# Optimization experiments

Measured on AMD Instinct MI355X. Metric: run time of the kernel, lower is better.

Reference implementation:

```python
import jax, jax.numpy as jnp
import numpy as np

N_NODES = 100000
N_EDGES = 600000
HID = 128
CH_OUT = 3


def setup_inputs() -> dict:
    key = jax.random.key(0)
    ks = jax.random.split(key, 16)
    s = 0.05  # small init to keep tanh in its linear-ish range
    inp = {
        "x": jax.random.normal(ks[0], (N_NODES, HID), dtype=jnp.float32),
        "pos": jax.random.normal(ks[1], (N_NODES, 3), dtype=jnp.float32),
        "edge_index": jax.random.randint(ks[2], (2, N_EDGES), 0, N_NODES, dtype=jnp.int32),
        "fe_w1": jax.random.normal(ks[3], (2 * HID + 1, HID), dtype=jnp.float32) * s,
        "fe_b1": jnp.zeros((HID,), jnp.float32),
        "fe_w2": jax.random.normal(ks[4], (HID, HID), dtype=jnp.float32) * s,
        "fe_b2": jnp.zeros((HID,), jnp.float32),
        "finf_w": jax.random.normal(ks[5], (HID, 1), dtype=jnp.float32) * s,
        "finf_b": jnp.zeros((1,), jnp.float32),
        "fh_w1": jax.random.normal(ks[6], (2 * HID, HID), dtype=jnp.float32) * s,
        "fh_b1": jnp.zeros((HID,), jnp.float32),
        "fh_w2": jax.random.normal(ks[7], (HID, HID), dtype=jnp.float32) * s,
        "fh_b2": jnp.zeros((HID,), jnp.float32),
        "l1_w": jax.random.normal(ks[8], (HID, HID), dtype=jnp.float32) * s,
        "l1_b": jnp.zeros((HID,), jnp.float32),
        "l2_w": jax.random.normal(ks[9], (HID, HID), dtype=jnp.float32) * s,
        "l2_b": jnp.zeros((HID,), jnp.float32),
        "l3_w": jax.random.normal(ks[10], (HID, HID), dtype=jnp.float32) * s,
        "l3_b": jnp.zeros((HID,), jnp.float32),
        "l4_w": jax.random.normal(ks[11], (HID, HID), dtype=jnp.float32) * s,
        "l4_b": jnp.zeros((HID,), jnp.float32),
        "l5_w": jax.random.normal(ks[12], (HID, CH_OUT), dtype=jnp.float32) * s,
        "l5_b": jnp.zeros((CH_OUT,), jnp.float32),
    }
    return inp


def reference(x, pos, edge_index, fe_w1, fe_b1, fe_w2, fe_b2, finf_w, finf_b,
              fh_w1, fh_b1, fh_w2, fh_b2, l1_w, l1_b, l2_w, l2_b, l3_w, l3_b,
              l4_w, l4_b, l5_w, l5_b):
    e_st, e_end = edge_index[0], edge_index[1]
    # dists = ||(pos_i - pos_j)^2||_2  (norm of the squared difference, as in source)
    d = pos[e_st] - pos[e_end]                                  # [E, 3]
    dists = jnp.linalg.norm(jnp.square(d), axis=1, keepdims=True)  # [E, 1]
    # edge MLP f_e
    tmp = jnp.concatenate([x[e_st], x[e_end], dists], axis=1)   # [E, 2H+1]
    m_ij = jnp.tanh(tmp @ fe_w1 + fe_b1)
    m_ij = jnp.tanh(m_ij @ fe_w2 + fe_b2)                        # [E, H]
    # gating f_inf
    e_ij = jnp.tanh(m_ij @ finf_w + finf_b)                      # [E, 1]
    # scatter-sum to source nodes (index_add on edge_index[0])
    m_i = jax.ops.segment_sum(e_ij * m_ij, e_st, num_segments=x.shape[0])  # [N, H]
    # node update f_h with residual
    h = jnp.concatenate([x, m_i], axis=1)                        # [N, 2H]
    x = x + (jnp.tanh(h @ fh_w1 + fh_b1) @ fh_w2 + fh_b2)
    # dense head (dropout p=0.0 is identity)
    lrelu = lambda v: jax.nn.leaky_relu(v, negative_slope=0.01)
    x = lrelu(x @ l1_w + l1_b)
    x = lrelu(x @ l2_w + l2_b)
    x = lrelu(x @ l3_w + l3_b)
    x = lrelu(x @ l4_w + l4_b)
    return x @ l5_w + l5_b
```

## Files before the change

kernel.cpp:

```cpp
#include <hip/hip_runtime.h>
#include <math.h>

#define HID 128

typedef unsigned short u16;
typedef __attribute__((ext_vector_type(8))) short bfrag;
typedef __attribute__((ext_vector_type(4))) float f32x4;
typedef __attribute__((ext_vector_type(8))) unsigned short u16x8;
typedef __attribute__((ext_vector_type(4))) unsigned short u16x4;

__device__ __forceinline__ float fast_tanh(float v) {
    v = fminf(15.0f, fmaxf(-15.0f, v));
    float e = __expf(2.0f * v);
    float r = __builtin_amdgcn_rcpf(e + 1.0f);
    return 1.0f - 2.0f * r;
}

__device__ __forceinline__ u16 f2b(float f) {
    union { float f; unsigned int u; } v;
    v.f = f;
    unsigned int u = v.u;
    return (u16)((u + 0x7FFFu + ((u >> 16) & 1u)) >> 16);
}
__device__ __forceinline__ float b2f(u16 b) {
    union { unsigned int u; float f; } v;
    v.u = ((unsigned int)b) << 16;
    return v.f;
}
__device__ __forceinline__ float bits2f(unsigned u) {
    union { unsigned u; float f; } v; v.u = u; return v.f;
}

__global__ void __launch_bounds__(256) prep_x(const float* __restrict__ x,
                                              u16* __restrict__ xb) {
    int i = blockIdx.x * 256 + threadIdx.x;
    const float4 v0 = *(const float4*)(x + (size_t)i * 8);
    const float4 v1 = *(const float4*)(x + (size_t)i * 8 + 4);
    u16x8 o = { f2b(v0.x), f2b(v0.y), f2b(v0.z), f2b(v0.w),
                f2b(v1.x), f2b(v1.y), f2b(v1.z), f2b(v1.w) };
    *(u16x8*)(xb + (size_t)i * 8) = o;
}

__global__ void __launch_bounds__(256) prep_weights(
    const float* __restrict__ w1, const float* __restrict__ fh1,
    const float* __restrict__ w2, const float* __restrict__ fh2,
    const float* __restrict__ l1, const float* __restrict__ l2,
    const float* __restrict__ l3, const float* __restrict__ l4,
    u16* __restrict__ w1t, u16* __restrict__ fh1t,
    u16* __restrict__ w2t, u16* __restrict__ fh2t,
    u16* __restrict__ l1t, u16* __restrict__ l2t,
    u16* __restrict__ l3t, u16* __restrict__ l4t)
{
    int b = blockIdx.x, t = threadIdx.x;
    const float* src; u16* dst; int K;
    if (b < 256) {
        K = 256;
        if (b < 128) { src = w1;  dst = w1t; }
        else         { src = fh1; dst = fh1t; b -= 128; }
    } else {
        K = 128;
        int s = (b - 256) >> 6; b = (b - 256) & 63;
        switch (s) {
            case 0:  src = w2;  dst = w2t;  break;
            case 1:  src = fh2; dst = fh2t; break;
            case 2:  src = l1;  dst = l1t;  break;
            case 3:  src = l2;  dst = l2t;  break;
            case 4:  src = l3;  dst = l3t;  break;
            default: src = l4;  dst = l4t;  break;
        }
    }
    int idx = b * 256 + t;
    int k = idx >> 7, n = idx & 127;
    dst[(size_t)n * K + k] = f2b(src[(size_t)k * 128 + n]);
}

__global__ void __launch_bounds__(256) hist_kernel(const int* __restrict__ est,
                                                   int* __restrict__ cnt, int E) {
    int e = blockIdx.x * 256 + threadIdx.x;
    if (e < E) atomicAdd(&cnt[est[e]], 1);
}

__global__ void __launch_bounds__(256) scan1(const int* __restrict__ cnt,
                                             int* __restrict__ scanout,
                                             int* __restrict__ partial, int N) {
    __shared__ int s[256];
    int t = threadIdx.x, b = blockIdx.x, i = b * 256 + t;
    int v = (i < N) ? cnt[i] : 0;
    s[t] = v; __syncthreads();
#pragma unroll
    for (int d = 1; d < 256; d <<= 1) {
        int add = (t >= d) ? s[t - d] : 0;
        __syncthreads();
        s[t] += add;
        __syncthreads();
    }
    if (i < N) scanout[i] = s[t] - v;
    if (t == 255) partial[b] = s[255];
}

__global__ void __launch_bounds__(512) scan2(int* __restrict__ partial, int NB) {
    __shared__ int s[512];
    int t = threadIdx.x;
    int v = (t < NB) ? partial[t] : 0;
    s[t] = v; __syncthreads();
#pragma unroll
    for (int d = 1; d < 512; d <<= 1) {
        int add = (t >= d) ? s[t - d] : 0;
        __syncthreads();
        s[t] += add;
        __syncthreads();
    }
    if (t < NB) partial[t] = s[t] - v;
}

__global__ void __launch_bounds__(256) scan3(const int* __restrict__ scanout,
                                             const int* __restrict__ partial,
                                             int* __restrict__ offs,
                                             int* __restrict__ cur, int N, int E) {
    int t = threadIdx.x, b = blockIdx.x, i = b * 256 + t;
    if (i < N) { int o = scanout[i] + partial[b]; offs[i] = o; cur[i] = o; }
    if (i == 0) offs[N] = E;
}

__global__ void __launch_bounds__(256) reorder_kernel(const int* __restrict__ est,
                                                      const int* __restrict__ eend,
                                                      int* __restrict__ cur,
                                                      int* __restrict__ est_s,
                                                      int* __restrict__ eend_s, int E) {
    int e = blockIdx.x * 256 + threadIdx.x;
    if (e < E) {
        int s = est[e];
        int p = atomicAdd(&cur[s], 1);
        est_s[p]  = s;
        eend_s[p] = eend[e];
    }
}

template<int KD>
__device__ __forceinline__ void gemm_k(const u16* sbuf, const u16* __restrict__ wt,
                                       int w, int l16, int l4g, f32x4 (&acc)[2][2]) {
    const int RS = KD * 2;
#pragma unroll
    for (int k0 = 0; k0 < KD; k0 += 32) {
        const int kb = k0 * 2 + l4g * 16;
        bfrag a0 = *(const bfrag*)((const char*)sbuf +
                    (unsigned)((l16 * RS + kb) ^ ((l16 & 7) << 4)));
        bfrag a1 = *(const bfrag*)((const char*)sbuf +
                    (unsigned)(((16 + l16) * RS + kb) ^ ((l16 & 7) << 4)));
        bfrag b0 = *(const bfrag*)((const char*)wt + (size_t)(32 * w + l16) * RS + kb);
        bfrag b1 = *(const bfrag*)((const char*)wt + (size_t)(32 * w + 16 + l16) * RS + kb);
        acc[0][0] = __builtin_amdgcn_mfma_f32_16x16x32_bf16(a0, b0, acc[0][0], 0, 0, 0);
        acc[0][1] = __builtin_amdgcn_mfma_f32_16x16x32_bf16(a0, b1, acc[0][1], 0, 0, 0);
        acc[1][0] = __builtin_amdgcn_mfma_f32_16x16x32_bf16(a1, b0, acc[1][0], 0, 0, 0);
        acc[1][1] = __builtin_amdgcn_mfma_f32_16x16x32_bf16(a1, b1, acc[1][1], 0, 0, 0);
    }
}

template<int KD>
__device__ __forceinline__ void gemm_sw(const u16* act, const u16* __restrict__ wt,
                                        int w, int l16, int l4g, f32x4 (&acc)[2][2]) {
    const int RS = KD * 2;
#pragma unroll
    for (int k0 = 0; k0 < KD; k0 += 32) {
        const int kb = k0 * 2 + l4g * 16;
        bfrag wa0 = *(const bfrag*)((const char*)wt + (size_t)(32 * w + l16) * RS + kb);
        bfrag wa1 = *(const bfrag*)((const char*)wt + (size_t)(32 * w + 16 + l16) * RS + kb);
        bfrag be0 = *(const bfrag*)((const char*)act +
                    (unsigned)((l16 * RS + kb) ^ ((l16 & 7) << 4)));
        bfrag be1 = *(const bfrag*)((const char*)act +
                    (unsigned)(((16 + l16) * RS + kb) ^ ((l16 & 7) << 4)));
        acc[0][0] = __builtin_amdgcn_mfma_f32_16x16x32_bf16(wa0, be0, acc[0][0], 0, 0, 0);
        acc[0][1] = __builtin_amdgcn_mfma_f32_16x16x32_bf16(wa0, be1, acc[0][1], 0, 0, 0);
        acc[1][0] = __builtin_amdgcn_mfma_f32_16x16x32_bf16(wa1, be0, acc[1][0], 0, 0, 0);
        acc[1][1] = __builtin_amdgcn_mfma_f32_16x16x32_bf16(wa1, be1, acc[1][1], 0, 0, 0);
    }
}

__global__ void __launch_bounds__(256, 2)
egc_edge_csr(const u16* __restrict__ xb, const float* __restrict__ pos,
             const int* __restrict__ est_s, const int* __restrict__ eend_s,
             const u16* __restrict__ w1t, const float* __restrict__ w1last,
             const float* __restrict__ b1, const u16* __restrict__ w2t,
             const float* __restrict__ b2, const float* __restrict__ fw,
             const float* __restrict__ fb, u16* __restrict__ g,
             float* __restrict__ ev, int n_tiles)
{
    __shared__ __attribute__((aligned(16))) u16 a_sh[2][32 * 256];
    __shared__ __attribute__((aligned(16))) u16 m1_sh[32 * 128];
    __shared__ float red[32][17];
    __shared__ float dist_l[2][32];

    const int t = threadIdx.x, lane = t & 63, w = t >> 6;
    const int l16 = lane & 15, l4g = lane >> 4;
    const unsigned swz = (unsigned)((l16 & 7) << 4);

    bfrag wa10[8], wa11[8], w2f0[4], w2f1[4];
#pragma unroll
    for (int i = 0; i < 8; ++i) {
        int kb = i * 64 + l4g * 16;
        wa10[i] = *(const bfrag*)((const char*)w1t + (size_t)(32 * w + l16) * 512 + kb);
        wa11[i] = *(const bfrag*)((const char*)w1t + (size_t)(32 * w + 16 + l16) * 512 + kb);
    }
#pragma unroll
    for (int i = 0; i < 4; ++i) {
        int kb = i * 64 + l4g * 16;
        w2f0[i] = *(const bfrag*)((const char*)w2t + (size_t)(32 * w + l16) * 256 + kb);
        w2f1[i] = *(const bfrag*)((const char*)w2t + (size_t)(32 * w + 16 + l16) * 256 + kb);
    }
    float w1l_r[2][4], b1_r[2][4], b2_r[2][4], fw_r[2][4];
#pragma unroll
    for (int mi = 0; mi < 2; ++mi)
#pragma unroll
        for (int rg = 0; rg < 4; ++rg) {
            int n = 32 * w + 16 * mi + l4g * 4 + rg;
            w1l_r[mi][rg] = w1last[n];
            b1_r[mi][rg]  = b1[n];
            b2_r[mi][rg]  = b2[n];
            fw_r[mi][rg]  = fw[n];
        }
    const float fbv = fb[0];

    float4 sv0, sv1, sv2, sv3;
    float pax = 0, pay = 0, paz = 0, pbx = 0, pby = 0, pbz = 0;

#define EDGE_ISSUE(TILE) do {                                                  \
        int e0_ = (TILE) * 32;                                                 \
        { int f_ = t;       int e_ = f_ >> 5, q_ = f_ & 31; int ge_ = e0_ + e_;\
          int nd_ = (q_ < 16) ? est_s[ge_] : eend_s[ge_];                      \
          sv0 = *(const float4*)(xb + (size_t)nd_ * 128 + (q_ & 15) * 8); }    \
        { int f_ = t + 256; int e_ = f_ >> 5, q_ = f_ & 31; int ge_ = e0_ + e_;\
          int nd_ = (q_ < 16) ? est_s[ge_] : eend_s[ge_];                      \
          sv1 = *(const float4*)(xb + (size_t)nd_ * 128 + (q_ & 15) * 8); }    \
        { int f_ = t + 512; int e_ = f_ >> 5, q_ = f_ & 31; int ge_ = e0_ + e_;\
          int nd_ = (q_ < 16) ? est_s[ge_] : eend_s[ge_];                      \
          sv2 = *(const float4*)(xb + (size_t)nd_ * 128 + (q_ & 15) * 8); }    \
        { int f_ = t + 768; int e_ = f_ >> 5, q_ = f_ & 31; int ge_ = e0_ + e_;\
          int nd_ = (q_ < 16) ? est_s[ge_] : eend_s[ge_];                      \
          sv3 = *(const float4*)(xb + (size_t)nd_ * 128 + (q_ & 15) * 8); }    \
        if (t < 32) {                                                          \
            int ge_ = e0_ + t;                                                 \
            int a_ = est_s[ge_], b_ = eend_s[ge_];                             \
            pax = pos[a_ * 3]; pay = pos[a_ * 3 + 1]; paz = pos[a_ * 3 + 2];   \
            pbx = pos[b_ * 3]; pby = pos[b_ * 3 + 1]; pbz = pos[b_ * 3 + 2];   \
        }                                                                      \
    } while (0)

#define EDGE_COMMIT(BUF) do {                                                  \
        { int f_ = t;       int e_ = f_ >> 5, q_ = f_ & 31;                    \
          unsigned by_ = (unsigned)(e_ * 512 + q_ * 16) ^ (unsigned)((e_ & 7) << 4); \
          *(float4*)((char*)a_sh[BUF] + by_) = sv0; }                          \
        { int f_ = t + 256; int e_ = f_ >> 5, q_ = f_ & 31;                    \
          unsigned by_ = (unsigned)(e_ * 512 + q_ * 16) ^ (unsigned)((e_ & 7) << 4); \
          *(float4*)((char*)a_sh[BUF] + by_) = sv1; }                          \
        { int f_ = t + 512; int e_ = f_ >> 5, q_ = f_ & 31;                    \
          unsigned by_ = (unsigned)(e_ * 512 + q_ * 16) ^ (unsigned)((e_ & 7) << 4); \
          *(float4*)((char*)a_sh[BUF] + by_) = sv2; }                          \
        { int f_ = t + 768; int e_ = f_ >> 5, q_ = f_ & 31;                    \
          unsigned by_ = (unsigned)(e_ * 512 + q_ * 16) ^ (unsigned)((e_ & 7) << 4); \
          *(float4*)((char*)a_sh[BUF] + by_) = sv3; }                          \
        if (t < 32) {                                                          \
            float dx_ = pax - pbx, dy_ = pay - pby, dz_ = paz - pbz;           \
            dx_ *= dx_; dy_ *= dy_; dz_ *= dz_;                                \
            dist_l[BUF][t] = sqrtf(dx_ * dx_ + dy_ * dy_ + dz_ * dz_);         \
        }                                                                      \
    } while (0)

    int tile = blockIdx.x;
    EDGE_ISSUE(tile);
    int buf = 0;

    if (tile < n_tiles)
    while (true) {
        EDGE_COMMIT(buf);
        __syncthreads();
        int next = tile + gridDim.x;
        if (next < n_tiles) EDGE_ISSUE(next);
        const int e0 = tile * 32;

        {
            f32x4 acc[2][2] = {};
#pragma unroll
            for (int i = 0; i < 8; ++i) {
                int kb = i * 64 + l4g * 16;
                bfrag be0 = *(const bfrag*)((const char*)a_sh[buf] +
                            ((unsigned)(l16 * 512 + kb) ^ swz));
                bfrag be1 = *(const bfrag*)((const char*)a_sh[buf] +
                            ((unsigned)((16 + l16) * 512 + kb) ^ swz));
                acc[0][0] = __builtin_amdgcn_mfma_f32_16x16x32_bf16(wa10[i], be0, acc[0][0], 0, 0, 0);
                acc[0][1] = __builtin_amdgcn_mfma_f32_16x16x32_bf16(wa10[i], be1, acc[0][1], 0, 0, 0);
                acc[1][0] = __builtin_amdgcn_mfma_f32_16x16x32_bf16(wa11[i], be0, acc[1][0], 0, 0, 0);
                acc[1][1] = __builtin_amdgcn_mfma_f32_16x16x32_bf16(wa11[i], be1, acc[1][1], 0, 0, 0);
            }
            float de0 = dist_l[buf][l16];
            float de1 = dist_l[buf][16 + l16];
#pragma unroll
            for (int mi = 0; mi < 2; ++mi)
#pragma unroll
                for (int ni = 0; ni < 2; ++ni) {
                    float de = ni ? de1 : de0;
                    u16x4 pk;
#pragma unroll
                    for (int rg = 0; rg < 4; ++rg) {
                        float v = fast_tanh(acc[mi][ni][rg] + de * w1l_r[mi][rg] + b1_r[mi][rg]);
                        pk[rg] = f2b(v);
                    }
                    unsigned byte = ((unsigned)((16 * ni + l16) * 256 +
                                     (32 * w + 16 * mi + l4g * 4) * 2)) ^ swz;
                    *(u16x4*)((char*)m1_sh + byte) = pk;
                }
        }
        __syncthreads();

        {
            f32x4 acc[2][2] = {};
#pragma unroll
            for (int i = 0; i < 4; ++i) {
                int kb = i * 64 + l4g * 16;
                bfrag me0 = *(const bfrag*)((const char*)m1_sh +
                            ((unsigned)(l16 * 256 + kb) ^ swz));
                bfrag me1 = *(const bfrag*)((const char*)m1_sh +
                            ((unsigned)((16 + l16) * 256 + kb) ^ swz));
                acc[0][0] = __builtin_amdgcn_mfma_f32_16x16x32_bf16(w2f0[i], me0, acc[0][0], 0, 0, 0);
                acc[0][1] = __builtin_amdgcn_mfma_f32_16x16x32_bf16(w2f0[i], me1, acc[0][1], 0, 0, 0);
                acc[1][0] = __builtin_amdgcn_mfma_f32_16x16x32_bf16(w2f1[i], me0, acc[1][0], 0, 0, 0);
                acc[1][1] = __builtin_amdgcn_mfma_f32_16x16x32_bf16(w2f1[i], me1, acc[1][1], 0, 0, 0);
            }
            float part0 = 0.0f, part1 = 0.0f;
#pragma unroll
            for (int mi = 0; mi < 2; ++mi)
#pragma unroll
                for (int ni = 0; ni < 2; ++ni) {
                    u16x4 pk;
                    float ps = 0.0f;
#pragma unroll
                    for (int rg = 0; rg < 4; ++rg) {
                        float v = fast_tanh(acc[mi][ni][rg] + b2_r[mi][rg]);
                        ps += v * fw_r[mi][rg];
                        pk[rg] = f2b(v);
                    }
                    if (ni) part1 += ps; else part0 += ps;
                    int dstrow = e0 + 16 * ni + l16;
                    *(u16x4*)(g + (size_t)dstrow * 128 + (32 * w + 16 * mi + l4g * 4)) = pk;
                }
            red[l16][w * 4 + l4g]      = part0;
            red[16 + l16][w * 4 + l4g] = part1;
        }
        __syncthreads();

        if (t < 32) {
            float s = 0.0f;
#pragma unroll
            for (int j = 0; j < 16; ++j) s += red[t][j];
            ev[e0 + t] = fast_tanh(s + fbv);
        }

        tile = next; buf ^= 1;
        if (tile >= n_tiles) break;
    }
#undef EDGE_ISSUE
#undef EDGE_COMMIT
}

__global__ void __launch_bounds__(256, 8)
gather_seq(const u16* __restrict__ g, const float* __restrict__ ev,
           const int* __restrict__ offs, u16* __restrict__ m_i)
{
    const int lane = threadIdx.x & 63;
    const int half = lane >> 5;
    const int l32  = lane & 31;
    const int n = blockIdx.x * 4 + (threadIdx.x >> 6);
    const int beg = offs[n], end = offs[n + 1];
    float a0 = 0.0f, a1 = 0.0f, a2 = 0.0f, a3 = 0.0f;
    for (int e = beg + half; e < end; e += 2) {
        uint2 v = *(const uint2*)(g + (size_t)e * 128 + l32 * 4);
        float ee = ev[e];
        a0 += ee * bits2f(v.x << 16);
        a1 += ee * bits2f(v.x & 0xFFFF0000u);
        a2 += ee * bits2f(v.y << 16);
        a3 += ee * bits2f(v.y & 0xFFFF0000u);
    }
    a0 += __shfl_xor(a0, 32);
    a1 += __shfl_xor(a1, 32);
    a2 += __shfl_xor(a2, 32);
    a3 += __shfl_xor(a3, 32);
    if (half == 0) {
        uint2 o;
        o.x = (unsigned)f2b(a0) | ((unsigned)f2b(a1) << 16);
        o.y = (unsigned)f2b(a2) | ((unsigned)f2b(a3) << 16);
        *(uint2*)(m_i + (size_t)n * 128 + l32 * 4) = o;
    }
}

__global__ void __launch_bounds__(256, 3)
egc_edge_mfma(const u16* __restrict__ xb, const float* __restrict__ pos,
              const int* __restrict__ est, const int* __restrict__ eend,
              const u16* __restrict__ w1t, const float* __restrict__ w1last,
              const float* __restrict__ b1, const u16* __restrict__ w2t,
              const float* __restrict__ b2, const float* __restrict__ fw,
              const float* __restrict__ fb, float* __restrict__ m_i)
{
    __shared__ __attribute__((aligned(16))) u16 a_sh[32 * 256];
    __shared__ __attribute__((aligned(16))) u16 m1_sh[32 * 128];
    __shared__ float m2_sh[32][132];
    __shared__ float dist_l[32];
    __shared__ float ev_l[32];
    __shared__ int   st_l[32];

    const int t = threadIdx.x;
    const int e0 = blockIdx.x * 32;
    const int lane = t & 63;
    const int w = t >> 6;
    const int l16 = lane & 15, l4g = lane >> 4;

#pragma unroll
    for (int i = 0; i < 4; ++i) {
        int f = t + 256 * i;
        int e = f >> 5, q = f & 31;
        int ge = e0 + e;
        int node = (q < 16) ? est[ge] : eend[ge];
        float4 v = *(const float4*)(xb + (size_t)node * 128 + (q & 15) * 8);
        unsigned byte = (unsigned)(e * 512 + q * 16) ^ (unsigned)((e & 7) << 4);
        *(float4*)((char*)a_sh + byte) = v;
    }
    if (t < 32) {
        int ge = e0 + t;
        int a = est[ge], b = eend[ge];
        st_l[t] = a;
        float dx = pos[a * 3 + 0] - pos[b * 3 + 0];
        float dy = pos[a * 3 + 1] - pos[b * 3 + 1];
        float dz = pos[a * 3 + 2] - pos[b * 3 + 2];
        dx *= dx; dy *= dy; dz *= dz;
        dist_l[t] = sqrtf(dx * dx + dy * dy + dz * dz);
    }
    __syncthreads();

    {
        f32x4 acc[2][2] = {};
        gemm_k<256>(a_sh, w1t, w, l16, l4g, acc);
#pragma unroll
        for (int mi = 0; mi < 2; ++mi)
#pragma unroll
            for (int ni = 0; ni < 2; ++ni) {
                const int col = 32 * w + 16 * ni + l16;
                const float wl = w1last[col], bb = b1[col];
#pragma unroll
                for (int rg = 0; rg < 4; ++rg) {
                    const int row = 16 * mi + l4g * 4 + rg;
                    float v = fast_tanh(acc[mi][ni][rg] + dist_l[row] * wl + bb);
                    unsigned byte = (unsigned)((row * 256 + col * 2) ^ ((row & 7) << 4));
                    *(u16*)((char*)m1_sh + byte) = f2b(v);
                }
            }
    }
    __syncthreads();

    {
        f32x4 acc[2][2] = {};
        gemm_k<128>(m1_sh, w2t, w, l16, l4g, acc);
#pragma unroll
        for (int mi = 0; mi < 2; ++mi)
#pragma unroll
            for (int ni = 0; ni < 2; ++ni) {
                const int col = 32 * w + 16 * ni + l16;
                const float bb = b2[col];
#pragma unroll
                for (int rg = 0; rg < 4; ++rg) {
                    const int row = 16 * mi + l4g * 4 + rg;
                    m2_sh[row][col] = fast_tanh(acc[mi][ni][rg] + bb);
                }
            }
    }
    __syncthreads();

    if (t < 128) {
        int e = t >> 2, p = t & 3;
        float s = 0.0f;
#pragma unroll
        for (int k = 0; k < 32; ++k) s += m2_sh[e][p * 32 + k] * fw[p * 32 + k];
        s += __shfl_xor(s, 1);
        s += __shfl_xor(s, 2);
        if (p == 0) ev_l[e] = fast_tanh(s + fb[0]);
    }
    __syncthreads();

    {
        int e = t >> 3, l8 = t & 7;
        float ev = ev_l[e];
        size_t base = (size_t)st_l[e] * HID + l8;
#pragma unroll
        for (int i = 0; i < 16; ++i)
            unsafeAtomicAdd(m_i + base + 8 * i, ev * m2_sh[e][l8 + 8 * i]);
    }
}

#define NODE_LAYER_SW(SRC, KD, WT, BIAS, DST, ACT)                             \
    {                                                                          \
        f32x4 acc[2][2] = {};                                                  \
        gemm_sw<KD>(SRC, WT, w, l16, l4g, acc);                                \
        float bbr[2][4];                                                       \
        _Pragma("unroll")                                                      \
        for (int mi = 0; mi < 2; ++mi)                                         \
            _Pragma("unroll")                                                  \
            for (int rg = 0; rg < 4; ++rg)                                     \
                bbr[mi][rg] = (BIAS)[32 * w + 16 * mi + l4g * 4 + rg];         \
        _Pragma("unroll")                                                      \
        for (int mi = 0; mi < 2; ++mi)                                         \
            _Pragma("unroll")                                                  \
            for (int ni = 0; ni < 2; ++ni) {                                   \
                const int node = 16 * ni + l16;                                \
                const int ch = 32 * w + 16 * mi + l4g * 4;                     \
                u16x4 pk;                                                      \
                _Pragma("unroll")                                              \
                for (int rg = 0; rg < 4; ++rg) {                               \
                    float v = acc[mi][ni][rg] + bbr[mi][rg];                   \
                    ACT;                                                       \
                    pk[rg] = f2b(v);                                           \
                }                                                              \
                unsigned byte = ((unsigned)(node * 256 + ch * 2)) ^ swz;       \
                *(u16x4*)((char*)(DST) + byte) = pk;                           \
            }                                                                  \
    }

template<bool MIBF16>
__global__ void __launch_bounds__(256, 3)
egc_node_mfma(const u16* __restrict__ xb, const float* __restrict__ xf,
              const void* __restrict__ m_i,
              const u16* __restrict__ fh1t, const float* __restrict__ hb1,
              const u16* __restrict__ fh2t, const float* __restrict__ hb2,
              const u16* __restrict__ l1t, const float* __restrict__ l1b,
              const u16* __restrict__ l2t, const float* __restrict__ l2b,
              const u16* __restrict__ l3t, const float* __restrict__ l3b,
              const u16* __restrict__ l4t, const float* __restrict__ l4b,
              const float* __restrict__ l5w, const float* __restrict__ l5b,
              float* __restrict__ out)
{
    __shared__ __attribute__((aligned(16))) u16 a_sh[32 * 256];
    __shared__ __attribute__((aligned(16))) u16 bA[32 * 128];
    __shared__ __attribute__((aligned(16))) u16 bB[32 * 128];
    __shared__ float ff[32][132];

    const int t = threadIdx.x;
    const int n0 = blockIdx.x * 32;
    const int lane = t & 63;
    const int w = t >> 6;
    const int l16 = lane & 15, l4g = lane >> 4;
    const unsigned swz = (unsigned)((l16 & 7) << 4);

#pragma unroll
    for (int i = 0; i < 2; ++i) {
        int f = t + 256 * i;
        int n = f >> 4, q = f & 15;
        float4 v = *(const float4*)(xb + (size_t)(n0 + n) * 128 + q * 8);
        unsigned byte = (unsigned)((n * 512 + q * 16) ^ ((n & 7) << 4));
        *(float4*)((char*)a_sh + byte) = v;
    }
    if (MIBF16) {
#pragma unroll
        for (int i = 0; i < 2; ++i) {
            int f = t + 256 * i;
            int n = f >> 4, q = f & 15;
            float4 v = *(const float4*)((const u16*)m_i + (size_t)(n0 + n) * 128 + q * 8);
            unsigned byte = (unsigned)((n * 512 + 256 + q * 16) ^ ((n & 7) << 4));
            *(float4*)((char*)a_sh + byte) = v;
        }
    } else {
#pragma unroll
        for (int i = 0; i < 2; ++i) {
            int f = t + 256 * i;
            int n = f >> 4, q = f & 15;
            const float* src = (const float*)m_i + (size_t)(n0 + n) * 128 + q * 8;
            float4 v0 = *(const float4*)(src);
            float4 v1 = *(const float4*)(src + 4);
            u16x8 o = { f2b(v0.x), f2b(v0.y), f2b(v0.z), f2b(v0.w),
                        f2b(v1.x), f2b(v1.y), f2b(v1.z), f2b(v1.w) };
            unsigned byte = (unsigned)((n * 512 + 256 + q * 16) ^ ((n & 7) << 4));
            *(u16x8*)((char*)a_sh + byte) = o;
        }
    }
    __syncthreads();

    NODE_LAYER_SW(a_sh, 256, fh1t, hb1, bA, { v = fast_tanh(v); })
    __syncthreads();

    {
        f32x4 acc[2][2] = {};
        gemm_sw<128>(bA, fh2t, w, l16, l4g, acc);
        float bbr[2][4];
#pragma unroll
        for (int mi = 0; mi < 2; ++mi)
#pragma unroll
            for (int rg = 0; rg < 4; ++rg)
                bbr[mi][rg] = hb2[32 * w + 16 * mi + l4g * 4 + rg];
#pragma unroll
        for (int mi = 0; mi < 2; ++mi)
#pragma unroll
            for (int ni = 0; ni < 2; ++ni) {
                const int node = 16 * ni + l16;
                const int ch = 32 * w + 16 * mi + l4g * 4;
                float4 xr = *(const float4*)(xf + (size_t)(n0 + node) * 128 + ch);
                u16x4 pk;
                pk[0] = f2b(acc[mi][ni][0] + bbr[mi][0] + xr.x);
                pk[1] = f2b(acc[mi][ni][1] + bbr[mi][1] + xr.y);
                pk[2] = f2b(acc[mi][ni][2] + bbr[mi][2] + xr.z);
                pk[3] = f2b(acc[mi][ni][3] + bbr[mi][3] + xr.w);
                unsigned byte = ((unsigned)(node * 256 + ch * 2)) ^ swz;
                *(u16x4*)((char*)bB + byte) = pk;
            }
    }
    __syncthreads();

    NODE_LAYER_SW(bB, 128, l1t, l1b, bA, { v = v > 0.0f ? v : 0.01f * v; })
    __syncthreads();
    NODE_LAYER_SW(bA, 128, l2t, l2b, bB, { v = v > 0.0f ? v : 0.01f * v; })
    __syncthreads();
    NODE_LAYER_SW(bB, 128, l3t, l3b, bA, { v = v > 0.0f ? v : 0.01f * v; })
    __syncthreads();

    {
        f32x4 acc[2][2] = {};
        gemm_sw<128>(bA, l4t, w, l16, l4g, acc);
        float bbr[2][4];
#pragma unroll
        for (int mi = 0; mi < 2; ++mi)
#pragma unroll
            for (int rg = 0; rg < 4; ++rg)
                bbr[mi][rg] = l4b[32 * w + 16 * mi + l4g * 4 + rg];
#pragma unroll
        for (int mi = 0; mi < 2; ++mi)
#pragma unroll
            for (int ni = 0; ni < 2; ++ni) {
                const int node = 16 * ni + l16;
                const int ch = 32 * w + 16 * mi + l4g * 4;
                float4 o;
                float v0 = acc[mi][ni][0] + bbr[mi][0];
                float v1 = acc[mi][ni][1] + bbr[mi][1];
                float v2 = acc[mi][ni][2] + bbr[mi][2];
                float v3 = acc[mi][ni][3] + bbr[mi][3];
                o.x = v0 > 0.0f ? v0 : 0.01f * v0;
                o.y = v1 > 0.0f ? v1 : 0.01f * v1;
                o.z = v2 > 0.0f ? v2 : 0.01f * v2;
                o.w = v3 > 0.0f ? v3 : 0.01f * v3;
                *(float4*)(&ff[node][ch]) = o;
            }
    }
    __syncthreads();

    if (t < 96) {
        int n = t / 3, cc = t % 3;
        float s = l5b[cc];
#pragma unroll 8
        for (int k = 0; k < HID; ++k) s += ff[n][k] * l5w[k * 3 + cc];
        out[(size_t)(n0 + n) * 3 + cc] = s;
    }
}

extern "C" void kernel_launch(void* const* d_in, const int* in_sizes, int n_in,
                              void* d_out, int out_size, void* d_ws, size_t ws_size,
                              hipStream_t stream)
{
    const float* x      = (const float*)d_in[0];
    const float* pos    = (const float*)d_in[1];
    const int*   eidx   = (const int*)d_in[2];
    const float* fe_w1  = (const float*)d_in[3];
    const float* fe_b1  = (const float*)d_in[4];
    const float* fe_w2  = (const float*)d_in[5];
    const float* fe_b2  = (const float*)d_in[6];
    const float* finf_w = (const float*)d_in[7];
    const float* finf_b = (const float*)d_in[8];
    const float* fh_w1  = (const float*)d_in[9];
    const float* fh_b1  = (const float*)d_in[10];
    const float* fh_w2  = (const float*)d_in[11];
    const float* fh_b2  = (const float*)d_in[12];
    const float* l1w    = (const float*)d_in[13];
    const float* l1b    = (const float*)d_in[14];
    const float* l2w    = (const float*)d_in[15];
    const float* l2b    = (const float*)d_in[16];
    const float* l3w    = (const float*)d_in[17];
    const float* l3b    = (const float*)d_in[18];
    const float* l4w    = (const float*)d_in[19];
    const float* l4b    = (const float*)d_in[20];
    const float* l5w    = (const float*)d_in[21];
    const float* l5b    = (const float*)d_in[22];
    float* out = (float*)d_out;

    const int n_edges = in_sizes[2] / 2;
    const int n_nodes = in_sizes[0] / HID;
    const int nsb     = (n_nodes + 255) / 256;
    const int n_tiles = n_edges / 32;

    char* ws = (char*)d_ws;
    const bool use_csr = (ws_size >= 208800000ULL);

    if (use_csr) {
        u16* g     = (u16*)(ws + 0);
        u16* xb    = (u16*)(ws + 153600000);
        u16* m_i   = (u16*)(ws + 179200000);
        int* est_s  = (int*)(ws + 179200000);
        int* eend_s = (int*)(ws + 181600000);
        u16* w1t  = (u16*)(ws + 204800000);
        u16* w2t  = (u16*)(ws + 204865536);
        u16* fh1t = (u16*)(ws + 204898304);
        u16* fh2t = (u16*)(ws + 204963840);
        u16* l1t  = (u16*)(ws + 204996608);
        u16* l2t  = (u16*)(ws + 205029376);
        u16* l3t  = (u16*)(ws + 205062144);
        u16* l4t  = (u16*)(ws + 205094912);
        int* cnt  = (int*)(ws + 205127680);
        int* offs = (int*)(ws + 205527680);
        int* cur  = (int*)(ws + 205927696);
        float* ev = (float*)(ws + 206327696);
        int* part = (int*)(ws + 208727696);

        (void)hipMemsetAsync(cnt, 0, (size_t)n_nodes * sizeof(int), stream);
        prep_x<<<dim3((n_nodes * HID) / (256 * 8)), dim3(256), 0, stream>>>(x, xb);
        prep_weights<<<dim3(640), dim3(256), 0, stream>>>(
            fe_w1, fh_w1, fe_w2, fh_w2, l1w, l2w, l3w, l4w,
            w1t, fh1t, w2t, fh2t, l1t, l2t, l3t, l4t);

        hist_kernel<<<dim3((n_edges + 255) / 256), dim3(256), 0, stream>>>(eidx, cnt, n_edges);
        scan1<<<dim3(nsb), dim3(256), 0, stream>>>(cnt, cnt, part, n_nodes);
        scan2<<<dim3(1), dim3(512), 0, stream>>>(part, nsb);
        scan3<<<dim3(nsb), dim3(256), 0, stream>>>(cnt, part, offs, cur, n_nodes, n_edges);
        reorder_kernel<<<dim3((n_edges + 255) / 256), dim3(256), 0, stream>>>(
            eidx, eidx + n_edges, cur, est_s, eend_s, n_edges);

        egc_edge_csr<<<dim3(768), dim3(256), 0, stream>>>(
            xb, pos, est_s, eend_s, w1t, fe_w1 + (size_t)256 * HID, fe_b1,
            w2t, fe_b2, finf_w, finf_b, g, ev, n_tiles);

        gather_seq<<<dim3(n_nodes / 4), dim3(256), 0, stream>>>(g, ev, offs, m_i);

        egc_node_mfma<true><<<dim3(n_nodes / 32), dim3(256), 0, stream>>>(
            xb, x, m_i, fh1t, fh_b1, fh2t, fh_b2, l1t, l1b, l2t, l2b,
            l3t, l3b, l4t, l4b, l5w, l5b, out);
    } else {
        float* m_i = (float*)(ws + 0);
        u16* xb    = (u16*)(ws + 51200000);
        u16* w1t   = (u16*)(ws + 76800000);
        u16* w2t   = (u16*)(ws + 76865536);
        u16* fh1t  = (u16*)(ws + 76898304);
        u16* fh2t  = (u16*)(ws + 76963840);
        u16* l1t   = (u16*)(ws + 76996608);
        u16* l2t   = (u16*)(ws + 77029376);
        u16* l3t   = (u16*)(ws + 77062144);
        u16* l4t   = (u16*)(ws + 77094912);

        (void)hipMemsetAsync(m_i, 0, (size_t)n_nodes * HID * sizeof(float), stream);
        prep_x<<<dim3((n_nodes * HID) / (256 * 8)), dim3(256), 0, stream>>>(x, xb);
        prep_weights<<<dim3(640), dim3(256), 0, stream>>>(
            fe_w1, fh_w1, fe_w2, fh_w2, l1w, l2w, l3w, l4w,
            w1t, fh1t, w2t, fh2t, l1t, l2t, l3t, l4t);

        egc_edge_mfma<<<dim3(n_edges / 32), dim3(256), 0, stream>>>(
            xb, pos, eidx, eidx + n_edges, w1t, fe_w1 + (size_t)256 * HID, fe_b1,
            w2t, fe_b2, finf_w, finf_b, m_i);

        egc_node_mfma<false><<<dim3(n_nodes / 32), dim3(256), 0, stream>>>(
            xb, x, m_i, fh1t, fh_b1, fh2t, fh_b2, l1t, l1b, l2t, l2b,
            l3t, l3b, l4t, l4b, l5w, l5b, out);
    }
}
```

Before: 393.8 us.

## Fuse CSR segment gather into node MLP kernel and drop tanh clamp

The separate gather_seq kernel, which summed gated edge messages per node and wrote m_i to global memory, is removed. Each node block now performs the CSR segment sum itself, with each wave handling 8 nodes and writing the bf16 result straight into the swizzled shared A tile. This saves one launch and a global round trip of m_i. Other changes: the fminf/fmaxf clamp in fast_tanh is removed, and the edge kernel grid drops from 768 to 512 blocks. The fused gather is serialized per wave and may lengthen the node kernel's prologue. Without the clamp, large inputs rely on exp overflow to inf, which makes rcp return 0.

```diff
diff --git a/kernel.cpp b/kernel.cpp
--- a/kernel.cpp
+++ b/kernel.cpp
@@ -10,7 +10,6 @@
 typedef __attribute__((ext_vector_type(4))) unsigned short u16x4;
 
 __device__ __forceinline__ float fast_tanh(float v) {
-    v = fminf(15.0f, fmaxf(-15.0f, v));
     float e = __expf(2.0f * v);
     float r = __builtin_amdgcn_rcpf(e + 1.0f);
     return 1.0f - 2.0f * r;
@@ -361,36 +360,6 @@
 #undef EDGE_COMMIT
 }
 
-__global__ void __launch_bounds__(256, 8)
-gather_seq(const u16* __restrict__ g, const float* __restrict__ ev,
-           const int* __restrict__ offs, u16* __restrict__ m_i)
-{
-    const int lane = threadIdx.x & 63;
-    const int half = lane >> 5;
-    const int l32  = lane & 31;
-    const int n = blockIdx.x * 4 + (threadIdx.x >> 6);
-    const int beg = offs[n], end = offs[n + 1];
-    float a0 = 0.0f, a1 = 0.0f, a2 = 0.0f, a3 = 0.0f;
-    for (int e = beg + half; e < end; e += 2) {
-        uint2 v = *(const uint2*)(g + (size_t)e * 128 + l32 * 4);
-        float ee = ev[e];
-        a0 += ee * bits2f(v.x << 16);
-        a1 += ee * bits2f(v.x & 0xFFFF0000u);
-        a2 += ee * bits2f(v.y << 16);
-        a3 += ee * bits2f(v.y & 0xFFFF0000u);
-    }
-    a0 += __shfl_xor(a0, 32);
-    a1 += __shfl_xor(a1, 32);
-    a2 += __shfl_xor(a2, 32);
-    a3 += __shfl_xor(a3, 32);
-    if (half == 0) {
-        uint2 o;
-        o.x = (unsigned)f2b(a0) | ((unsigned)f2b(a1) << 16);
-        o.y = (unsigned)f2b(a2) | ((unsigned)f2b(a3) << 16);
-        *(uint2*)(m_i + (size_t)n * 128 + l32 * 4) = o;
-    }
-}
-
 __global__ void __launch_bounds__(256, 3)
 egc_edge_mfma(const u16* __restrict__ xb, const float* __restrict__ pos,
               const int* __restrict__ est, const int* __restrict__ eend,
@@ -521,10 +490,12 @@
             }                                                                  \
     }
 
-template<bool MIBF16>
+template<int MODE>
 __global__ void __launch_bounds__(256, 3)
 egc_node_mfma(const u16* __restrict__ xb, const float* __restrict__ xf,
               const void* __restrict__ m_i,
+              const u16* __restrict__ gbuf, const float* __restrict__ ev,
+              const int* __restrict__ offs,
               const u16* __restrict__ fh1t, const float* __restrict__ hb1,
               const u16* __restrict__ fh2t, const float* __restrict__ hb2,
               const u16* __restrict__ l1t, const float* __restrict__ l1b,
@@ -554,14 +525,34 @@
         unsigned byte = (unsigned)((n * 512 + q * 16) ^ ((n & 7) << 4));
         *(float4*)((char*)a_sh + byte) = v;
     }
-    if (MIBF16) {
-#pragma unroll
-        for (int i = 0; i < 2; ++i) {
-            int f = t + 256 * i;
-            int n = f >> 4, q = f & 15;
-            float4 v = *(const float4*)((const u16*)m_i + (size_t)(n0 + n) * 128 + q * 8);
-            unsigned byte = (unsigned)((n * 512 + 256 + q * 16) ^ ((n & 7) << 4));
-            *(float4*)((char*)a_sh + byte) = v;
+
+    if (MODE == 0) {
+        const int half = lane >> 5;
+        const int l32  = lane & 31;
+#pragma unroll 1
+        for (int j = 0; j < 8; ++j) {
+            const int r = 8 * w + j;
+            const int n = n0 + r;
+            const int beg = offs[n], end = offs[n + 1];
+            float a0 = 0.0f, a1 = 0.0f, a2 = 0.0f, a3 = 0.0f;
+            for (int e = beg + half; e < end; e += 2) {
+                uint2 v = *(const uint2*)(gbuf + (size_t)e * 128 + l32 * 4);
+                float ee = ev[e];
+                a0 += ee * bits2f(v.x << 16);
+                a1 += ee * bits2f(v.x & 0xFFFF0000u);
+                a2 += ee * bits2f(v.y << 16);
+                a3 += ee * bits2f(v.y & 0xFFFF0000u);
+            }
+            a0 += __shfl_xor(a0, 32);
+            a1 += __shfl_xor(a1, 32);
+            a2 += __shfl_xor(a2, 32);
+            a3 += __shfl_xor(a3, 32);
+            if (half == 0) {
+                u16x4 pk = { f2b(a0), f2b(a1), f2b(a2), f2b(a3) };
+                unsigned byte = ((unsigned)(r * 512 + 256 + l32 * 8)) ^
+                                (unsigned)((r & 7) << 4);
+                *(u16x4*)((char*)a_sh + byte) = pk;
+            }
         }
     } else {
 #pragma unroll
@@ -694,7 +685,6 @@
     if (use_csr) {
         u16* g     = (u16*)(ws + 0);
         u16* xb    = (u16*)(ws + 153600000);
-        u16* m_i   = (u16*)(ws + 179200000);
         int* est_s  = (int*)(ws + 179200000);
         int* eend_s = (int*)(ws + 181600000);
         u16* w1t  = (u16*)(ws + 204800000);
@@ -724,14 +714,12 @@
         reorder_kernel<<<dim3((n_edges + 255) / 256), dim3(256), 0, stream>>>(
             eidx, eidx + n_edges, cur, est_s, eend_s, n_edges);
 
-        egc_edge_csr<<<dim3(768), dim3(256), 0, stream>>>(
+        egc_edge_csr<<<dim3(512), dim3(256), 0, stream>>>(
             xb, pos, est_s, eend_s, w1t, fe_w1 + (size_t)256 * HID, fe_b1,
             w2t, fe_b2, finf_w, finf_b, g, ev, n_tiles);
 
-        gather_seq<<<dim3(n_nodes / 4), dim3(256), 0, stream>>>(g, ev, offs, m_i);
-
-        egc_node_mfma<true><<<dim3(n_nodes / 32), dim3(256), 0, stream>>>(
-            xb, x, m_i, fh1t, fh_b1, fh2t, fh_b2, l1t, l1b, l2t, l2b,
+        egc_node_mfma<0><<<dim3(n_nodes / 32), dim3(256), 0, stream>>>(
+            xb, x, nullptr, g, ev, offs, fh1t, fh_b1, fh2t, fh_b2, l1t, l1b, l2t, l2b,
             l3t, l3b, l4t, l4b, l5w, l5b, out);
     } else {
         float* m_i = (float*)(ws + 0);
@@ -755,8 +743,8 @@
             xb, pos, eidx, eidx + n_edges, w1t, fe_w1 + (size_t)256 * HID, fe_b1,
             w2t, fe_b2, finf_w, finf_b, m_i);
 
-        egc_node_mfma<false><<<dim3(n_nodes / 32), dim3(256), 0, stream>>>(
-            xb, x, m_i, fh1t, fh_b1, fh2t, fh_b2, l1t, l1b, l2t, l2b,
-            l3t, l3b, l4t, l4b, l5w, l5b, out);
-    }
-}
+        egc_node_mfma<1><<<dim3(n_nodes / 32), dim3(256), 0, stream>>>(
+            xb, x, m_i, nullptr, nullptr, nullptr, fh1t, fh_b1, fh2t, fh_b2,
+            l1t, l1b, l2t, l2b, l3t, l3b, l4t, l4b, l5w, l5b, out);
+    }
+}
```

After: 395.2 us. No clear change (+0.4%).
